# Kernel tuning notes

Measured on AMD Instinct MI355X. Metric: run time of the kernel, lower is better.

The kernel has to match this reference:

```python
import jax, jax.numpy as jnp
import numpy as np

jax.config.update("jax_enable_x64", True)  # original torch code runs in float64; minors underflow fp32

D = 96   # Nsites
N = 48   # Nparticles


def setup_inputs() -> dict:
    key = jax.random.key(0)
    # Orthonormal single-particle orbitals (columns), as the module assumes (P^T P = I)
    A = jax.random.normal(key, (D, D), dtype=jnp.float64)
    Q, _ = jnp.linalg.qr(A)
    P = Q[:, :N]  # [D, N]
    # A valid ordered particle configuration: strictly increasing, occ_positions[k] <= D-N+k
    occ_positions = jnp.arange(N, dtype=jnp.int32) * (D // N)  # stride-2 filling
    return {"P": P, "occ_positions": occ_positions}


def _cond_probs(P, occ_positions):
    """Conditional probabilities probs[k, x] of placing the k-th (ordered) particle at
    site x given particles 0..k-1 at occ_positions[0..k-1].

    Math identical to SlaterDetSampler_ordered.get_cond_prob (naive_update=True):
      G = I - P P^T
      probs[k,x] = -det(M_x[0:x+1,0:x+1]) / det(M[0:xmin,0:xmin])
    where M = G - diag(occupancy of particles < k) and M_x additionally sets n_x = 1.
    Since Ksites is always the contiguous range 0..x, all determinants are LEADING
    principal minors; and because only the (x,x) diagonal entry changes by -1 (last index
    of the block), det(M_x block) = d_{x+1} - d_x with d_j the leading j-minor of M.
    """
    Dd, Nn = P.shape
    dt = P.dtype
    eye = jnp.eye(Dd, dtype=dt)
    G = eye - P @ P.T                                             # [D, D]

    onehots = jax.nn.one_hot(occ_positions, Dd, dtype=dt)         # [N, D]
    n_before = jnp.cumsum(onehots, axis=0) - onehots              # occupancy of particles < k
    A = G[None] - n_before[:, :, None] * eye                      # [N, D, D]: G - diag(n_<k)

    # All leading principal minors via batched det of masked matrices:
    # M_j = A on the [0:j,0:j] block, identity elsewhere  =>  det(M_j) = leading j-minor
    ii = jnp.arange(Dd)
    jj = jnp.arange(1, Dd + 1)
    blk = (ii[None, :, None] < jj[:, None, None]) & (ii[None, None, :] < jj[:, None, None])  # [D,D,D]
    Ms = jnp.where(blk[None], A[:, None], eye)                    # [N, D, D, D]
    d = jnp.linalg.det(Ms.reshape(Nn * Dd, Dd, Dd)).reshape(Nn, Dd)
    d_full = jnp.concatenate([jnp.ones((Nn, 1), dt), d], axis=1)  # d_full[k, j] = j-th leading minor

    k = jnp.arange(Nn)
    xmin = jnp.where(k == 0, 0, occ_positions[jnp.maximum(k - 1, 0)] + 1)  # [N]
    xmax = Dd - Nn + k + 1                                                  # [N]
    denom = jnp.take_along_axis(d_full, xmin[:, None], axis=1)              # [N, 1]
    num = d_full[:, 1:] - d_full[:, :-1]                                    # det(GG_num) per candidate x

    x = jnp.arange(Dd)
    support = (x[None, :] >= xmin[:, None]) & (x[None, :] < xmax[:, None])
    probs = jnp.where(support, -num / denom, jnp.zeros((), dt))
    # torch.where(abs(probs) > 1e-15, probs, 0.)
    probs = jnp.where(jnp.abs(probs) > 1e-15, probs, jnp.zeros((), dt))
    return probs


def reference(P, occ_positions):
    probs = _cond_probs(P, occ_positions)                          # [N, D]
    # prob of the full ordered sample = prod_k probs[k, occ_positions[k]]  (as in sample())
    p_k = jnp.take_along_axis(probs, occ_positions[:, None], axis=1)[:, 0]
    prob_sample = jnp.prod(p_k)
    return probs, prob_sample
```

## Files before the change

kernel.cpp:

```cpp
#include <hip/hip_runtime.h>
#include <math.h>

#define Dd 96
#define Nn 48
#define LD 97
#define PTS 98

__device__ __forceinline__ double frcp(double x) {
    double r = __builtin_amdgcn_rcp(x);
    r = fma(fma(-x, r, 1.0), r, r);
    r = fma(fma(-x, r, 1.0), r, r);
    return r;
}

__device__ __forceinline__ double rdlane(double v, int srcLane) {
    union { double d; int i[2]; } u; u.d = v;
    int lo = __builtin_amdgcn_readlane(u.i[0], srcLane);
    int hi = __builtin_amdgcn_readlane(u.i[1], srcLane);
    union { int i[2]; double d; } w; w.i[0] = lo; w.i[1] = hi;
    return w.d;
}

__global__ __launch_bounds__(1024, 1) void slater_kernel(const float* __restrict__ P,
                                                         const int* __restrict__ occ,
                                                         float* __restrict__ out,
                                                         unsigned* __restrict__ cnt) {
    __shared__ double As[Dd * LD];
    __shared__ double Sbuf[4][6][Dd];
    __shared__ double ev16[16][6];
    __shared__ int    evmask16[16], sdead16[16];
    __shared__ double evm[6];
    __shared__ int    evmmask;
    __shared__ double gs_runprod;
    __shared__ int    gs_dead;
    __shared__ int    step_pub;
    __shared__ int    done4[4];
    __shared__ unsigned char flag[Dd];
    float* PT = (float*)As;

    const int tid  = threadIdx.x;
    const int k    = blockIdx.x;
    const int n    = Dd - Nn + k + 1;
    const int lane = tid & 63;
    const int wave = tid >> 6;
    const int xmin = (k == 0) ? 0 : occ[k - 1] + 1;
    const int s_end = (n - 1) / 6;
    const int jend  = 6 * s_end;

    if (tid == 0) { step_pub = -1; gs_runprod = 1.0; gs_dead = 0; evmmask = 0; }
    if (tid < 4)  done4[tid] = 0;
    if (tid < 16) { evmask16[tid] = 0; sdead16[tid] = 0; }
    if (tid < Dd) flag[tid] = 0;
    __syncthreads();
    if (tid < k) flag[occ[tid]] = 1;
    for (int e = tid; e < Dd * Nn; e += 1024) {
        int c = e / Nn, t = e - (e / Nn) * Nn;
        PT[t * PTS + c] = P[e];
    }
    __syncthreads();

    double Areg[8]; int trs[2], tcs[2];
#pragma unroll
    for (int it = 0; it < 2; ++it) {
        int tau = tid + 1024 * it;
        double s00 = 0.0, s01 = 0.0, s10 = 0.0, s11 = 0.0;
        int tr = 0, tc = 0;
        if (tau < 1176) {
            tr = (int)((97.0 - sqrt(9409.0 - 8.0 * (double)tau)) * 0.5);
            while ((tr * (97 - tr)) / 2 > tau) --tr;
            while (((tr + 1) * (96 - tr)) / 2 <= tau) ++tr;
            tc = tr + (tau - (tr * (97 - tr)) / 2);
            int r0 = 2 * tr, c0 = 2 * tc;
            if (r0 < n && c0 < n) {
                for (int t = 0; t < Nn; ++t) {
                    const float* row = PT + t * PTS;
                    float2 pr = *(const float2*)(row + r0);
                    float2 pc = *(const float2*)(row + c0);
                    s00 -= (double)pr.x * (double)pc.x; s01 -= (double)pr.x * (double)pc.y;
                    s10 -= (double)pr.y * (double)pc.x; s11 -= (double)pr.y * (double)pc.y;
                }
            }
        }
        trs[it] = tr; tcs[it] = tc;
        Areg[it * 4 + 0] = s00; Areg[it * 4 + 1] = s01;
        Areg[it * 4 + 2] = s10; Areg[it * 4 + 3] = s11;
    }
    __syncthreads();
#pragma unroll
    for (int it = 0; it < 2; ++it) {
        int tau = tid + 1024 * it;
        if (tau < 1176) {
            int tr = trs[it], tc = tcs[it];
            int r0 = 2 * tr, c0 = 2 * tc;
            if (r0 < n && c0 < n) {
                bool r1 = (r0 + 1 < n), c1 = (c0 + 1 < n);
                double d0 = flag[r0] ? 0.0 : 1.0;
                double d1 = flag[r0 + 1] ? 0.0 : 1.0;
                As[r0 * LD + c0] = Areg[it * 4 + 0] + ((r0 == c0) ? d0 : 0.0);
                if (c1)       As[r0 * LD + c0 + 1]       = Areg[it * 4 + 1];
                if (r1)       As[(r0 + 1) * LD + c0]     = Areg[it * 4 + 2];
                if (r1 && c1) As[(r0 + 1) * LD + c0 + 1] = Areg[it * 4 + 3] + ((r0 == c0) ? d1 : 0.0);
                if (tr != tc) {
                    As[c0 * LD + r0] = Areg[it * 4 + 0];
                    if (c1)       As[(c0 + 1) * LD + r0]     = Areg[it * 4 + 1];
                    if (r1)       As[c0 * LD + r0 + 1]       = Areg[it * 4 + 2];
                    if (r1 && c1) As[(c0 + 1) * LD + r0 + 1] = Areg[it * 4 + 3];
                }
            }
        }
    }
    __syncthreads();

    double myprob = 0.0;
    double rr[6][2];

#pragma unroll
    for (int u = 0; u < 6; ++u) {
        if (lane < 48) {
            rr[u][0] = As[(6 * wave + u) * LD + 2 * lane];
            rr[u][1] = As[(6 * wave + u) * LD + 2 * lane + 1];
        } else { rr[u][0] = 0.0; rr[u][1] = 0.0; }
    }

    auto prefactor = [&](int p, int slot) {
        const int jb = 6 * p, jbH = 3 * p;
        double grun = gs_runprod; int gdead = gs_dead;
        int msk = 0;
#pragma unroll
        for (int cc = 0; cc < 6; ++cc) {
            const int src = jbH + (cc >> 1);
            double piv = rdlane(rr[cc][cc & 1], src);
            if (!gdead) {
                double ap = fabs(piv);
                int jj = jb + cc;
                if (jj >= xmin) {
                    if (lane == 0) ev16[p][cc] = grun * (1.0 - piv);
                    msk |= (1 << cc);
                    double nr = grun * piv;
                    if (!(ap > 1e-7) || !(ap < 8.0) || !(fabs(nr) > 1e-8)) gdead = 1;
                    else grun = nr;
                } else {
                    if (!(ap > 1e-12) || !(ap < 8.0)) gdead = 1;
                }
            }
            double rp = frcp(piv);
            rr[cc][0] *= rp; rr[cc][1] *= rp;
#pragma unroll
            for (int i = 0; i < 6; ++i) {
                if (i == cc) continue;
                double f = rdlane(rr[i][cc & 1], src);
                rr[i][0] -= f * rr[cc][0];
                rr[i][1] -= f * rr[cc][1];
            }
        }
        if (lane == 0) {
            evmask16[p] = msk; sdead16[p] = gdead;
            gs_runprod = grun; gs_dead = gdead;
        }
        if (lane < 48) {
            const bool live = (2 * lane >= jb + 6);
#pragma unroll
            for (int r = 0; r < 6; ++r) {
                double2 sv;
                sv.x = live ? rr[r][0] : 0.0;
                sv.y = live ? rr[r][1] : 0.0;
                *(double2*)&Sbuf[slot][r][2 * lane] = sv;
            }
        }
        __threadfence_block();
        if (lane == 0)
            __hip_atomic_store(&step_pub, p, __ATOMIC_RELEASE, __HIP_MEMORY_SCOPE_WORKGROUP);
    };

    if (wave == 0) prefactor(0, 0);

    bool broke = false;
    const int smax = (wave < s_end) ? wave : s_end;
    for (int s = 0; s < smax; ++s) {
        while (__hip_atomic_load(&step_pub, __ATOMIC_ACQUIRE,
                                 __HIP_MEMORY_SCOPE_WORKGROUP) < s)
            __builtin_amdgcn_s_sleep(1);
        if (sdead16[s]) { broke = true; break; }
        const int slot = s & 3;
        double S0[6], S1[6];
        if (lane < 48) {
#pragma unroll
            for (int r = 0; r < 6; ++r) {
                double2 sv = *(const double2*)&Sbuf[slot][r][2 * lane];
                S0[r] = sv.x; S1[r] = sv.y;
            }
        }
        asm volatile("s_waitcnt lgkmcnt(0)" ::: "memory");
        if (lane == 0)
            __hip_atomic_fetch_add(&done4[slot], 1, __ATOMIC_RELAXED,
                                   __HIP_MEMORY_SCOPE_WORKGROUP);
        if (lane < 48) {
            const int al = 3 * s;
#pragma unroll
            for (int u = 0; u < 6; ++u) {
#pragma unroll
                for (int r = 0; r < 6; ++r) {
                    double a = rdlane(rr[u][r & 1], al + (r >> 1));
                    rr[u][0] -= a * S0[r];
                    rr[u][1] -= a * S1[r];
                }
            }
        }
        if (wave == s + 1 && s + 1 < s_end) {
            const int p = s + 1;
            if (p >= 4) {
                const int q = p & 3, m = p >> 2;
                const int T = m * (15 - q) - 2 * m * (m - 1);
                while (__hip_atomic_load(&done4[q], __ATOMIC_ACQUIRE,
                                         __HIP_MEMORY_SCOPE_WORKGROUP) < T)
                    __builtin_amdgcn_s_sleep(1);
            }
            prefactor(p, p & 3);
        }
    }

    if (!broke && wave == s_end) {
        const int rsz = n - jend;
        double grun = gs_runprod; int gdead = gs_dead;
        int msk = 0;
#pragma unroll
        for (int cc = 0; cc < 6; ++cc) {
            const int src = 3 * s_end + (cc >> 1);
            double piv = rdlane(rr[cc][cc & 1], src);
            double evv = 0.0;
            if (cc < rsz - 1) {
                if (!gdead) {
                    double ap = fabs(piv);
                    int jj = jend + cc;
                    if (jj >= xmin) {
                        evv = grun * (1.0 - piv); msk |= (1 << cc);
                        double nr = grun * piv;
                        if (!(ap > 1e-7) || !(ap < 8.0) || !(fabs(nr) > 1e-8)) gdead = 1;
                        else grun = nr;
                    } else {
                        if (!(ap > 1e-12) || !(ap < 8.0)) gdead = 1;
                    }
                }
            } else if (cc == rsz - 1) {
                if (!gdead) { evv = grun * (1.0 - piv); msk |= (1 << cc); }
            }
            if (lane == 0) evm[cc] = evv;
            double rp = frcp(piv);
            rr[cc][0] *= rp; rr[cc][1] *= rp;
#pragma unroll
            for (int i = 0; i < 6; ++i) {
                if (i == cc) continue;
                double f = rdlane(rr[i][cc & 1], src);
                rr[i][0] -= f * rr[cc][0];
                rr[i][1] -= f * rr[cc][1];
            }
        }
        if (lane == 0) evmmask = msk;
    }
    __syncthreads();

    if (tid < jend) {
        int sp = tid / 6, q = tid - 6 * sp;
        if ((evmask16[sp] >> q) & 1) myprob = ev16[sp][q];
    } else if (tid < n) {
        int q = tid - jend;
        if ((evmmask >> q) & 1) myprob = evm[q];
    }

    if (tid < Dd) {
        double p = myprob;
        if (!isfinite(p)) p = 0.0;
        if (!(fabs(p) > 1e-15)) p = 0.0;
        p = fmin(fmax(p, 0.0), 1.0);
        out[k * Dd + tid] = (float)p;
    }

    __threadfence();
    __syncthreads();
    if (wave == 0) {
        int old = 0;
        if (lane == 0)
            old = (int)__hip_atomic_fetch_add(cnt, 1u, __ATOMIC_ACQ_REL,
                                              __HIP_MEMORY_SCOPE_AGENT);
        old = __shfl(old, 0, 64);
        if (((unsigned)old + 1u) % (unsigned)Nn == 0u) {
            __threadfence();
            double v = 1.0;
            if (lane < Nn) {
                float f = __hip_atomic_load(out + lane * Dd + occ[lane],
                                            __ATOMIC_RELAXED, __HIP_MEMORY_SCOPE_AGENT);
                v = (double)f;
            }
#pragma unroll
            for (int off = 32; off >= 1; off >>= 1)
                v *= __shfl_down(v, off, 64);
            if (lane == 0) {
                if (!isfinite(v)) v = 0.0;
                out[Nn * Dd] = (float)v;
            }
        }
    }
}

extern "C" void kernel_launch(void* const* d_in, const int* in_sizes, int n_in,
                              void* d_out, int out_size, void* d_ws, size_t ws_size,
                              hipStream_t stream) {
    const float* P = (const float*)d_in[0];
    const int* occ = (const int*)d_in[1];
    float* out = (float*)d_out;

    slater_kernel<<<Nn, 1024, 0, stream>>>(P, occ, out, (unsigned*)d_ws);
}
```

Before: 96.03 us.

## Compute -P P^T once in a separate kernel and share across blocks

Splits the monolithic kernel into a small build_g kernel that computes -P·P^T once into workspace, followed by an elimination kernel that reads rows straight from global memory into registers. This removes the redundant per-block GEMM and the shared-memory staging and transpose of the matrix that each of the 48 blocks did before. It adds a second launch and a global round trip of a 96x96 double matrix. The old kernel is kept as a fallback when the workspace is too small.

```diff
diff --git a/kernel.cpp b/kernel.cpp
--- a/kernel.cpp
+++ b/kernel.cpp
@@ -5,6 +5,7 @@
 #define Nn 48
 #define LD 97
 #define PTS 98
+#define WS_G_BYTES (Dd * Dd * 8)
 
 __device__ __forceinline__ double frcp(double x) {
     double r = __builtin_amdgcn_rcp(x);
@@ -21,10 +22,254 @@
     return w.d;
 }
 
-__global__ __launch_bounds__(1024, 1) void slater_kernel(const float* __restrict__ P,
-                                                         const int* __restrict__ occ,
-                                                         float* __restrict__ out,
-                                                         unsigned* __restrict__ cnt) {
+__global__ __launch_bounds__(256) void build_g(const float* __restrict__ P,
+                                               double* __restrict__ Mg) {
+    __shared__ float Ps[Dd * 48];
+    const int t0 = threadIdx.x;
+    for (int e = t0; e < Dd * 48; e += 256) Ps[e] = P[e];
+    __syncthreads();
+    const int e = blockIdx.x * 256 + t0;
+    const int r = e / Dd, c = e - Dd * (e / Dd);
+    const float* pr = Ps + r * 48;
+    const float* pc = Ps + c * 48;
+    double acc = 0.0;
+#pragma unroll
+    for (int t = 0; t < 48; ++t)
+        acc -= (double)pr[t] * (double)pc[t];
+    Mg[e] = acc;
+}
+
+__global__ __launch_bounds__(1024, 1) void slater_elim(const double* __restrict__ Mg,
+                                                       const int* __restrict__ occ,
+                                                       float* __restrict__ out,
+                                                       unsigned* __restrict__ cnt) {
+    __shared__ double Sbuf[4][6][Dd];
+    __shared__ double ev16[16][6];
+    __shared__ int    evmask16[16], sdead16[16];
+    __shared__ double evm[6];
+    __shared__ int    evmmask;
+    __shared__ double gs_runprod;
+    __shared__ int    gs_dead;
+    __shared__ int    step_pub;
+    __shared__ int    done4[4];
+    __shared__ unsigned char flag[Dd];
+
+    const int tid  = threadIdx.x;
+    const int k    = blockIdx.x;
+    const int n    = Dd - Nn + k + 1;
+    const int lane = tid & 63;
+    const int wave = tid >> 6;
+    const int xmin = (k == 0) ? 0 : occ[k - 1] + 1;
+    const int s_end = (n - 1) / 6;
+    const int jend  = 6 * s_end;
+
+    if (tid == 0) { step_pub = -1; gs_runprod = 1.0; gs_dead = 0; evmmask = 0; }
+    if (tid < 4)  done4[tid] = 0;
+    if (tid < 16) { evmask16[tid] = 0; sdead16[tid] = 0; }
+    if (tid < Dd) flag[tid] = 0;
+    __syncthreads();
+    if (tid < k) flag[occ[tid]] = 1;
+    __syncthreads();
+
+    double myprob = 0.0;
+    double rr[6][2];
+
+#pragma unroll
+    for (int u = 0; u < 6; ++u) {
+        if (lane < 48) {
+            const int row = 6 * wave + u;
+            double2 g = *(const double2*)(Mg + row * Dd + 2 * lane);
+            double d0 = (row == 2 * lane     && !flag[row]) ? 1.0 : 0.0;
+            double d1 = (row == 2 * lane + 1 && !flag[row]) ? 1.0 : 0.0;
+            rr[u][0] = g.x + d0;
+            rr[u][1] = g.y + d1;
+        } else { rr[u][0] = 0.0; rr[u][1] = 0.0; }
+    }
+
+    auto prefactor = [&](int p, int slot) {
+        const int jb = 6 * p, jbH = 3 * p;
+        double grun = gs_runprod; int gdead = gs_dead;
+        int msk = 0;
+#pragma unroll
+        for (int cc = 0; cc < 6; ++cc) {
+            const int src = jbH + (cc >> 1);
+            double piv = rdlane(rr[cc][cc & 1], src);
+            if (!gdead) {
+                double ap = fabs(piv);
+                int jj = jb + cc;
+                if (jj >= xmin) {
+                    if (lane == 0) ev16[p][cc] = grun * (1.0 - piv);
+                    msk |= (1 << cc);
+                    double nr = grun * piv;
+                    if (!(ap > 1e-7) || !(ap < 8.0) || !(fabs(nr) > 1e-8)) gdead = 1;
+                    else grun = nr;
+                } else {
+                    if (!(ap > 1e-12) || !(ap < 8.0)) gdead = 1;
+                }
+            }
+            double rp = frcp(piv);
+            rr[cc][0] *= rp; rr[cc][1] *= rp;
+#pragma unroll
+            for (int i = 0; i < 6; ++i) {
+                if (i == cc) continue;
+                double f = rdlane(rr[i][cc & 1], src);
+                rr[i][0] -= f * rr[cc][0];
+                rr[i][1] -= f * rr[cc][1];
+            }
+        }
+        if (lane == 0) {
+            evmask16[p] = msk; sdead16[p] = gdead;
+            gs_runprod = grun; gs_dead = gdead;
+        }
+        if (lane < 48) {
+            const bool live = (2 * lane >= jb + 6);
+#pragma unroll
+            for (int r = 0; r < 6; ++r) {
+                double2 sv;
+                sv.x = live ? rr[r][0] : 0.0;
+                sv.y = live ? rr[r][1] : 0.0;
+                *(double2*)&Sbuf[slot][r][2 * lane] = sv;
+            }
+        }
+        __threadfence_block();
+        if (lane == 0)
+            __hip_atomic_store(&step_pub, p, __ATOMIC_RELEASE, __HIP_MEMORY_SCOPE_WORKGROUP);
+    };
+
+    if (wave == 0) prefactor(0, 0);
+
+    bool broke = false;
+    const int smax = (wave < s_end) ? wave : s_end;
+    for (int s = 0; s < smax; ++s) {
+        while (__hip_atomic_load(&step_pub, __ATOMIC_ACQUIRE,
+                                 __HIP_MEMORY_SCOPE_WORKGROUP) < s)
+            __builtin_amdgcn_s_sleep(1);
+        if (sdead16[s]) { broke = true; break; }
+        const int slot = s & 3;
+        double S0[6], S1[6];
+        if (lane < 48) {
+#pragma unroll
+            for (int r = 0; r < 6; ++r) {
+                double2 sv = *(const double2*)&Sbuf[slot][r][2 * lane];
+                S0[r] = sv.x; S1[r] = sv.y;
+            }
+        }
+        asm volatile("s_waitcnt lgkmcnt(0)" ::: "memory");
+        if (lane == 0)
+            __hip_atomic_fetch_add(&done4[slot], 1, __ATOMIC_RELAXED,
+                                   __HIP_MEMORY_SCOPE_WORKGROUP);
+        if (lane < 48) {
+            const int al = 3 * s;
+#pragma unroll
+            for (int u = 0; u < 6; ++u) {
+#pragma unroll
+                for (int r = 0; r < 6; ++r) {
+                    double a = rdlane(rr[u][r & 1], al + (r >> 1));
+                    rr[u][0] -= a * S0[r];
+                    rr[u][1] -= a * S1[r];
+                }
+            }
+        }
+        if (wave == s + 1 && s + 1 < s_end) {
+            const int p = s + 1;
+            if (p >= 4) {
+                const int q = p & 3, m = p >> 2;
+                const int T = m * (15 - q) - 2 * m * (m - 1);
+                while (__hip_atomic_load(&done4[q], __ATOMIC_ACQUIRE,
+                                         __HIP_MEMORY_SCOPE_WORKGROUP) < T)
+                    __builtin_amdgcn_s_sleep(1);
+            }
+            prefactor(p, p & 3);
+        }
+    }
+
+    if (!broke && wave == s_end) {
+        const int rsz = n - jend;
+        double grun = gs_runprod; int gdead = gs_dead;
+        int msk = 0;
+#pragma unroll
+        for (int cc = 0; cc < 6; ++cc) {
+            const int src = 3 * s_end + (cc >> 1);
+            double piv = rdlane(rr[cc][cc & 1], src);
+            double evv = 0.0;
+            if (cc < rsz - 1) {
+                if (!gdead) {
+                    double ap = fabs(piv);
+                    int jj = jend + cc;
+                    if (jj >= xmin) {
+                        evv = grun * (1.0 - piv); msk |= (1 << cc);
+                        double nr = grun * piv;
+                        if (!(ap > 1e-7) || !(ap < 8.0) || !(fabs(nr) > 1e-8)) gdead = 1;
+                        else grun = nr;
+                    } else {
+                        if (!(ap > 1e-12) || !(ap < 8.0)) gdead = 1;
+                    }
+                }
+            } else if (cc == rsz - 1) {
+                if (!gdead) { evv = grun * (1.0 - piv); msk |= (1 << cc); }
+            }
+            if (lane == 0) evm[cc] = evv;
+            double rp = frcp(piv);
+            rr[cc][0] *= rp; rr[cc][1] *= rp;
+#pragma unroll
+            for (int i = 0; i < 6; ++i) {
+                if (i == cc) continue;
+                double f = rdlane(rr[i][cc & 1], src);
+                rr[i][0] -= f * rr[cc][0];
+                rr[i][1] -= f * rr[cc][1];
+            }
+        }
+        if (lane == 0) evmmask = msk;
+    }
+    __syncthreads();
+
+    if (tid < jend) {
+        int sp = tid / 6, q = tid - 6 * sp;
+        if ((evmask16[sp] >> q) & 1) myprob = ev16[sp][q];
+    } else if (tid < n) {
+        int q = tid - jend;
+        if ((evmmask >> q) & 1) myprob = evm[q];
+    }
+
+    if (tid < Dd) {
+        double p = myprob;
+        if (!isfinite(p)) p = 0.0;
+        if (!(fabs(p) > 1e-15)) p = 0.0;
+        p = fmin(fmax(p, 0.0), 1.0);
+        out[k * Dd + tid] = (float)p;
+    }
+
+    __threadfence();
+    __syncthreads();
+    if (wave == 0) {
+        int old = 0;
+        if (lane == 0)
+            old = (int)__hip_atomic_fetch_add(cnt, 1u, __ATOMIC_ACQ_REL,
+                                              __HIP_MEMORY_SCOPE_AGENT);
+        old = __shfl(old, 0, 64);
+        if (((unsigned)old + 1u) % (unsigned)Nn == 0u) {
+            __threadfence();
+            double v = 1.0;
+            if (lane < Nn) {
+                float f = __hip_atomic_load(out + lane * Dd + occ[lane],
+                                            __ATOMIC_RELAXED, __HIP_MEMORY_SCOPE_AGENT);
+                v = (double)f;
+            }
+#pragma unroll
+            for (int off = 32; off >= 1; off >>= 1)
+                v *= __shfl_down(v, off, 64);
+            if (lane == 0) {
+                if (!isfinite(v)) v = 0.0;
+                out[Nn * Dd] = (float)v;
+            }
+        }
+    }
+}
+
+__global__ __launch_bounds__(1024, 1) void slater_mono(const float* __restrict__ P,
+                                                       const int* __restrict__ occ,
+                                                       float* __restrict__ out,
+                                                       unsigned* __restrict__ cnt) {
     __shared__ double As[Dd * LD];
     __shared__ double Sbuf[4][6][Dd];
     __shared__ double ev16[16][6];
@@ -113,7 +358,6 @@
 
     double myprob = 0.0;
     double rr[6][2];
-
 #pragma unroll
     for (int u = 0; u < 6; ++u) {
         if (lane < 48) {
@@ -309,5 +553,12 @@
     const int* occ = (const int*)d_in[1];
     float* out = (float*)d_out;
 
-    slater_kernel<<<Nn, 1024, 0, stream>>>(P, occ, out, (unsigned*)d_ws);
+    if (ws_size >= (size_t)(WS_G_BYTES + 16)) {
+        double* Mg = (double*)d_ws;
+        unsigned* cnt = (unsigned*)((char*)d_ws + WS_G_BYTES);
+        build_g<<<36, 256, 0, stream>>>(P, Mg);
+        slater_elim<<<Nn, 1024, 0, stream>>>(Mg, occ, out, cnt);
+    } else {
+        slater_mono<<<Nn, 1024, 0, stream>>>(P, occ, out, (unsigned*)d_ws);
+    }
 }
```

Result: faster. 93.64 us (-2.5%).

## Fuse Gram build into per-wave registers and drop shared matrix staging

Applied to the files above, without the earlier changes.

Each wave now computes its own 6-row slab of G = I - P P^T directly from global P with float4 loads. This replaces transposing P into shared memory, building the full symmetric matrix there, and reloading rows from it. Removing those steps cuts two block-wide barriers and a large shared array. The panel buffer grows to one slot per step, so the done-counter back-pressure handshake disappears. Other changes: the next-owner wave spins without sleep at raised priority, inactive waves skip work, and the update of row cc+1 is hoisted so the next pivot is ready sooner. The cost is redundant global reads of P across waves and a larger shared panel buffer.

```diff
diff --git a/kernel.cpp b/kernel.cpp
--- a/kernel.cpp
+++ b/kernel.cpp
@@ -3,8 +3,6 @@
 
 #define Dd 96
 #define Nn 48
-#define LD 97
-#define PTS 98
 
 __device__ __forceinline__ double frcp(double x) {
     double r = __builtin_amdgcn_rcp(x);
@@ -21,12 +19,11 @@
     return w.d;
 }
 
-__global__ __launch_bounds__(1024, 1) void slater_kernel(const float* __restrict__ P,
-                                                         const int* __restrict__ occ,
-                                                         float* __restrict__ out,
-                                                         unsigned* __restrict__ cnt) {
-    __shared__ double As[Dd * LD];
-    __shared__ double Sbuf[4][6][Dd];
+__global__ __launch_bounds__(1024, 1) void slater_fused(const float* __restrict__ P,
+                                                        const int* __restrict__ occ,
+                                                        float* __restrict__ out,
+                                                        unsigned* __restrict__ cnt) {
+    __shared__ double Sbuf[16][6][Dd];
     __shared__ double ev16[16][6];
     __shared__ int    evmask16[16], sdead16[16];
     __shared__ double evm[6];
@@ -34,9 +31,7 @@
     __shared__ double gs_runprod;
     __shared__ int    gs_dead;
     __shared__ int    step_pub;
-    __shared__ int    done4[4];
     __shared__ unsigned char flag[Dd];
-    float* PT = (float*)As;
 
     const int tid  = threadIdx.x;
     const int k    = blockIdx.x;
@@ -48,192 +43,66 @@
     const int jend  = 6 * s_end;
 
     if (tid == 0) { step_pub = -1; gs_runprod = 1.0; gs_dead = 0; evmmask = 0; }
-    if (tid < 4)  done4[tid] = 0;
     if (tid < 16) { evmask16[tid] = 0; sdead16[tid] = 0; }
     if (tid < Dd) flag[tid] = 0;
     __syncthreads();
     if (tid < k) flag[occ[tid]] = 1;
-    for (int e = tid; e < Dd * Nn; e += 1024) {
-        int c = e / Nn, t = e - (e / Nn) * Nn;
-        PT[t * PTS + c] = P[e];
-    }
-    __syncthreads();
-
-    double Areg[8]; int trs[2], tcs[2];
-#pragma unroll
-    for (int it = 0; it < 2; ++it) {
-        int tau = tid + 1024 * it;
-        double s00 = 0.0, s01 = 0.0, s10 = 0.0, s11 = 0.0;
-        int tr = 0, tc = 0;
-        if (tau < 1176) {
-            tr = (int)((97.0 - sqrt(9409.0 - 8.0 * (double)tau)) * 0.5);
-            while ((tr * (97 - tr)) / 2 > tau) --tr;
-            while (((tr + 1) * (96 - tr)) / 2 <= tau) ++tr;
-            tc = tr + (tau - (tr * (97 - tr)) / 2);
-            int r0 = 2 * tr, c0 = 2 * tc;
-            if (r0 < n && c0 < n) {
-                for (int t = 0; t < Nn; ++t) {
-                    const float* row = PT + t * PTS;
-                    float2 pr = *(const float2*)(row + r0);
-                    float2 pc = *(const float2*)(row + c0);
-                    s00 -= (double)pr.x * (double)pc.x; s01 -= (double)pr.x * (double)pc.y;
-                    s10 -= (double)pr.y * (double)pc.x; s11 -= (double)pr.y * (double)pc.y;
-                }
-            }
-        }
-        trs[it] = tr; tcs[it] = tc;
-        Areg[it * 4 + 0] = s00; Areg[it * 4 + 1] = s01;
-        Areg[it * 4 + 2] = s10; Areg[it * 4 + 3] = s11;
-    }
-    __syncthreads();
-#pragma unroll
-    for (int it = 0; it < 2; ++it) {
-        int tau = tid + 1024 * it;
-        if (tau < 1176) {
-            int tr = trs[it], tc = tcs[it];
-            int r0 = 2 * tr, c0 = 2 * tc;
-            if (r0 < n && c0 < n) {
-                bool r1 = (r0 + 1 < n), c1 = (c0 + 1 < n);
-                double d0 = flag[r0] ? 0.0 : 1.0;
-                double d1 = flag[r0 + 1] ? 0.0 : 1.0;
-                As[r0 * LD + c0] = Areg[it * 4 + 0] + ((r0 == c0) ? d0 : 0.0);
-                if (c1)       As[r0 * LD + c0 + 1]       = Areg[it * 4 + 1];
-                if (r1)       As[(r0 + 1) * LD + c0]     = Areg[it * 4 + 2];
-                if (r1 && c1) As[(r0 + 1) * LD + c0 + 1] = Areg[it * 4 + 3] + ((r0 == c0) ? d1 : 0.0);
-                if (tr != tc) {
-                    As[c0 * LD + r0] = Areg[it * 4 + 0];
-                    if (c1)       As[(c0 + 1) * LD + r0]     = Areg[it * 4 + 1];
-                    if (r1)       As[c0 * LD + r0 + 1]       = Areg[it * 4 + 2];
-                    if (r1 && c1) As[(c0 + 1) * LD + r0 + 1] = Areg[it * 4 + 3];
-                }
-            }
-        }
-    }
     __syncthreads();
 
     double myprob = 0.0;
     double rr[6][2];
-
-#pragma unroll
-    for (int u = 0; u < 6; ++u) {
+    const bool active = (wave <= s_end);
+
+    if (active) {
+        double acc[6][2];
+#pragma unroll
+        for (int u = 0; u < 6; ++u) { acc[u][0] = 0.0; acc[u][1] = 0.0; }
         if (lane < 48) {
-            rr[u][0] = As[(6 * wave + u) * LD + 2 * lane];
-            rr[u][1] = As[(6 * wave + u) * LD + 2 * lane + 1];
-        } else { rr[u][0] = 0.0; rr[u][1] = 0.0; }
-    }
-
-    auto prefactor = [&](int p, int slot) {
-        const int jb = 6 * p, jbH = 3 * p;
-        double grun = gs_runprod; int gdead = gs_dead;
-        int msk = 0;
-#pragma unroll
-        for (int cc = 0; cc < 6; ++cc) {
-            const int src = jbH + (cc >> 1);
-            double piv = rdlane(rr[cc][cc & 1], src);
-            if (!gdead) {
-                double ap = fabs(piv);
-                int jj = jb + cc;
-                if (jj >= xmin) {
-                    if (lane == 0) ev16[p][cc] = grun * (1.0 - piv);
-                    msk |= (1 << cc);
-                    double nr = grun * piv;
-                    if (!(ap > 1e-7) || !(ap < 8.0) || !(fabs(nr) > 1e-8)) gdead = 1;
-                    else grun = nr;
-                } else {
-                    if (!(ap > 1e-12) || !(ap < 8.0)) gdead = 1;
-                }
-            }
-            double rp = frcp(piv);
-            rr[cc][0] *= rp; rr[cc][1] *= rp;
-#pragma unroll
-            for (int i = 0; i < 6; ++i) {
-                if (i == cc) continue;
-                double f = rdlane(rr[i][cc & 1], src);
-                rr[i][0] -= f * rr[cc][0];
-                rr[i][1] -= f * rr[cc][1];
-            }
-        }
-        if (lane == 0) {
-            evmask16[p] = msk; sdead16[p] = gdead;
-            gs_runprod = grun; gs_dead = gdead;
-        }
-        if (lane < 48) {
-            const bool live = (2 * lane >= jb + 6);
-#pragma unroll
-            for (int r = 0; r < 6; ++r) {
-                double2 sv;
-                sv.x = live ? rr[r][0] : 0.0;
-                sv.y = live ? rr[r][1] : 0.0;
-                *(double2*)&Sbuf[slot][r][2 * lane] = sv;
-            }
-        }
-        __threadfence_block();
-        if (lane == 0)
-            __hip_atomic_store(&step_pub, p, __ATOMIC_RELEASE, __HIP_MEMORY_SCOPE_WORKGROUP);
-    };
-
-    if (wave == 0) prefactor(0, 0);
-
-    bool broke = false;
-    const int smax = (wave < s_end) ? wave : s_end;
-    for (int s = 0; s < smax; ++s) {
-        while (__hip_atomic_load(&step_pub, __ATOMIC_ACQUIRE,
-                                 __HIP_MEMORY_SCOPE_WORKGROUP) < s)
-            __builtin_amdgcn_s_sleep(1);
-        if (sdead16[s]) { broke = true; break; }
-        const int slot = s & 3;
-        double S0[6], S1[6];
-        if (lane < 48) {
-#pragma unroll
-            for (int r = 0; r < 6; ++r) {
-                double2 sv = *(const double2*)&Sbuf[slot][r][2 * lane];
-                S0[r] = sv.x; S1[r] = sv.y;
-            }
-        }
-        asm volatile("s_waitcnt lgkmcnt(0)" ::: "memory");
-        if (lane == 0)
-            __hip_atomic_fetch_add(&done4[slot], 1, __ATOMIC_RELAXED,
-                                   __HIP_MEMORY_SCOPE_WORKGROUP);
-        if (lane < 48) {
-            const int al = 3 * s;
-#pragma unroll
-            for (int u = 0; u < 6; ++u) {
-#pragma unroll
-                for (int r = 0; r < 6; ++r) {
-                    double a = rdlane(rr[u][r & 1], al + (r >> 1));
-                    rr[u][0] -= a * S0[r];
-                    rr[u][1] -= a * S1[r];
-                }
-            }
-        }
-        if (wave == s + 1 && s + 1 < s_end) {
-            const int p = s + 1;
-            if (p >= 4) {
-                const int q = p & 3, m = p >> 2;
-                const int T = m * (15 - q) - 2 * m * (m - 1);
-                while (__hip_atomic_load(&done4[q], __ATOMIC_ACQUIRE,
-                                         __HIP_MEMORY_SCOPE_WORKGROUP) < T)
-                    __builtin_amdgcn_s_sleep(1);
-            }
-            prefactor(p, p & 3);
-        }
-    }
-
-    if (!broke && wave == s_end) {
-        const int rsz = n - jend;
-        double grun = gs_runprod; int gdead = gs_dead;
-        int msk = 0;
-#pragma unroll
-        for (int cc = 0; cc < 6; ++cc) {
-            const int src = 3 * s_end + (cc >> 1);
-            double piv = rdlane(rr[cc][cc & 1], src);
-            double evv = 0.0;
-            if (cc < rsz - 1) {
+            const float* pc0 = P + (2 * lane) * 48;
+            const float* pc1 = pc0 + 48;
+            const float* pr0 = P + (6 * wave) * 48;
+            for (int t4 = 0; t4 < 12; ++t4) {
+                float4 v0 = ((const float4*)pc0)[t4];
+                float4 v1 = ((const float4*)pc1)[t4];
+#pragma unroll
+                for (int u = 0; u < 6; ++u) {
+                    float4 vr = ((const float4*)(pr0 + u * 48))[t4];
+                    acc[u][0] -= (double)vr.x * (double)v0.x;
+                    acc[u][0] -= (double)vr.y * (double)v0.y;
+                    acc[u][0] -= (double)vr.z * (double)v0.z;
+                    acc[u][0] -= (double)vr.w * (double)v0.w;
+                    acc[u][1] -= (double)vr.x * (double)v1.x;
+                    acc[u][1] -= (double)vr.y * (double)v1.y;
+                    acc[u][1] -= (double)vr.z * (double)v1.z;
+                    acc[u][1] -= (double)vr.w * (double)v1.w;
+                }
+            }
+        }
+#pragma unroll
+        for (int u = 0; u < 6; ++u) {
+            if (lane < 48) {
+                const int row = 6 * wave + u;
+                double d0 = (row == 2 * lane     && !flag[row]) ? 1.0 : 0.0;
+                double d1 = (row == 2 * lane + 1 && !flag[row]) ? 1.0 : 0.0;
+                rr[u][0] = acc[u][0] + d0;
+                rr[u][1] = acc[u][1] + d1;
+            } else { rr[u][0] = 0.0; rr[u][1] = 0.0; }
+        }
+
+        auto prefactor = [&](int p) {
+            const int jb = 6 * p, jbH = 3 * p;
+            double grun = gs_runprod; int gdead = gs_dead;
+            int msk = 0;
+#pragma unroll
+            for (int cc = 0; cc < 6; ++cc) {
+                const int src = jbH + (cc >> 1);
+                double piv = rdlane(rr[cc][cc & 1], src);
                 if (!gdead) {
                     double ap = fabs(piv);
-                    int jj = jend + cc;
+                    int jj = jb + cc;
                     if (jj >= xmin) {
-                        evv = grun * (1.0 - piv); msk |= (1 << cc);
+                        if (lane == 0) ev16[p][cc] = grun * (1.0 - piv);
+                        msk |= (1 << cc);
                         double nr = grun * piv;
                         if (!(ap > 1e-7) || !(ap < 8.0) || !(fabs(nr) > 1e-8)) gdead = 1;
                         else grun = nr;
@@ -241,21 +110,122 @@
                         if (!(ap > 1e-12) || !(ap < 8.0)) gdead = 1;
                     }
                 }
-            } else if (cc == rsz - 1) {
-                if (!gdead) { evv = grun * (1.0 - piv); msk |= (1 << cc); }
-            }
-            if (lane == 0) evm[cc] = evv;
-            double rp = frcp(piv);
-            rr[cc][0] *= rp; rr[cc][1] *= rp;
-#pragma unroll
-            for (int i = 0; i < 6; ++i) {
-                if (i == cc) continue;
-                double f = rdlane(rr[i][cc & 1], src);
-                rr[i][0] -= f * rr[cc][0];
-                rr[i][1] -= f * rr[cc][1];
-            }
-        }
-        if (lane == 0) evmmask = msk;
+                double rp = frcp(piv);
+                rr[cc][0] *= rp; rr[cc][1] *= rp;
+                if (cc < 5) {
+                    double f = rdlane(rr[cc + 1][cc & 1], src);
+                    rr[cc + 1][0] -= f * rr[cc][0];
+                    rr[cc + 1][1] -= f * rr[cc][1];
+                }
+#pragma unroll
+                for (int i = 0; i < 6; ++i) {
+                    if (i == cc || i == cc + 1) continue;
+                    double f = rdlane(rr[i][cc & 1], src);
+                    rr[i][0] -= f * rr[cc][0];
+                    rr[i][1] -= f * rr[cc][1];
+                }
+            }
+            if (lane == 0) {
+                evmask16[p] = msk; sdead16[p] = gdead;
+                gs_runprod = grun; gs_dead = gdead;
+            }
+            if (lane < 48) {
+                const bool live = (2 * lane >= jb + 6);
+#pragma unroll
+                for (int r = 0; r < 6; ++r) {
+                    double2 sv;
+                    sv.x = live ? rr[r][0] : 0.0;
+                    sv.y = live ? rr[r][1] : 0.0;
+                    *(double2*)&Sbuf[p][r][2 * lane] = sv;
+                }
+            }
+            __threadfence_block();
+            if (lane == 0)
+                __hip_atomic_store(&step_pub, p, __ATOMIC_RELEASE, __HIP_MEMORY_SCOPE_WORKGROUP);
+        };
+
+        if (wave == 0) prefactor(0);
+
+        bool broke = false;
+        const int smax = (wave < s_end) ? wave : s_end;
+        for (int s = 0; s < smax; ++s) {
+            const bool nextOwner = (wave == s + 1);
+            if (nextOwner) {
+                while (__hip_atomic_load(&step_pub, __ATOMIC_ACQUIRE,
+                                         __HIP_MEMORY_SCOPE_WORKGROUP) < s) {}
+            } else {
+                while (__hip_atomic_load(&step_pub, __ATOMIC_ACQUIRE,
+                                         __HIP_MEMORY_SCOPE_WORKGROUP) < s)
+                    __builtin_amdgcn_s_sleep(2);
+            }
+            if (sdead16[s]) { broke = true; break; }
+            if (nextOwner) __builtin_amdgcn_s_setprio(1);
+            double S0[6], S1[6];
+            if (lane < 48) {
+#pragma unroll
+                for (int r = 0; r < 6; ++r) {
+                    double2 sv = *(const double2*)&Sbuf[s][r][2 * lane];
+                    S0[r] = sv.x; S1[r] = sv.y;
+                }
+                const int al = 3 * s;
+#pragma unroll
+                for (int u = 0; u < 6; ++u) {
+#pragma unroll
+                    for (int r = 0; r < 6; ++r) {
+                        double a = rdlane(rr[u][r & 1], al + (r >> 1));
+                        rr[u][0] -= a * S0[r];
+                        rr[u][1] -= a * S1[r];
+                    }
+                }
+            }
+            if (nextOwner && s + 1 < s_end)
+                prefactor(s + 1);
+            if (nextOwner) __builtin_amdgcn_s_setprio(0);
+        }
+
+        if (!broke && wave == s_end) {
+            const int rsz = n - jend;
+            double grun = gs_runprod; int gdead = gs_dead;
+            int msk = 0;
+#pragma unroll
+            for (int cc = 0; cc < 6; ++cc) {
+                const int src = 3 * s_end + (cc >> 1);
+                double piv = rdlane(rr[cc][cc & 1], src);
+                double evv = 0.0;
+                if (cc < rsz - 1) {
+                    if (!gdead) {
+                        double ap = fabs(piv);
+                        int jj = jend + cc;
+                        if (jj >= xmin) {
+                            evv = grun * (1.0 - piv); msk |= (1 << cc);
+                            double nr = grun * piv;
+                            if (!(ap > 1e-7) || !(ap < 8.0) || !(fabs(nr) > 1e-8)) gdead = 1;
+                            else grun = nr;
+                        } else {
+                            if (!(ap > 1e-12) || !(ap < 8.0)) gdead = 1;
+                        }
+                    }
+                } else if (cc == rsz - 1) {
+                    if (!gdead) { evv = grun * (1.0 - piv); msk |= (1 << cc); }
+                }
+                if (lane == 0) evm[cc] = evv;
+                double rp = frcp(piv);
+                rr[cc][0] *= rp; rr[cc][1] *= rp;
+                if (cc < 5) {
+                    double f = rdlane(rr[cc + 1][cc & 1], src);
+                    rr[cc + 1][0] -= f * rr[cc][0];
+                    rr[cc + 1][1] -= f * rr[cc][1];
+                }
+#pragma unroll
+                for (int i = 0; i < 6; ++i) {
+                    if (i == cc || i == cc + 1) continue;
+                    double f = rdlane(rr[i][cc & 1], src);
+                    rr[i][0] -= f * rr[cc][0];
+                    rr[i][1] -= f * rr[cc][1];
+                }
+            }
+            if (lane == 0) evmmask = msk;
+        }
     }
     __syncthreads();
 
@@ -309,5 +279,5 @@
     const int* occ = (const int*)d_in[1];
     float* out = (float*)d_out;
 
-    slater_kernel<<<Nn, 1024, 0, stream>>>(P, occ, out, (unsigned*)d_ws);
-}
+    slater_fused<<<Nn, 1024, 0, stream>>>(P, occ, out, (unsigned*)d_ws);
+}
```

Measured after the change: 98.51 us. 2.6% more time.
